# Performance work log

Measured on AMD Instinct MI355X. Metric: run time of the kernel, lower is better.

Reference implementation:

```python
import jax, jax.numpy as jnp
import numpy as np

EMB_DIM = 64
B, S, D = 64, 1024, 64

def setup_inputs() -> dict:
    key = jax.random.key(0)
    k1, k2, k3, k4, k5 = jax.random.split(key, 5)
    return {
        "query": jax.random.normal(k1, (B, S, D), dtype=jnp.float32),
        "key": jax.random.normal(k2, (B, S, D), dtype=jnp.float32),
        "value": jax.random.normal(k3, (B, S, D), dtype=jnp.float32),
        "a_key": jax.random.normal(k4, (S, S, D), dtype=jnp.float32),
        "a_value": jax.random.normal(k5, (S, S, D), dtype=jnp.float32),
    }

def reference(query, key, value, a_key, a_value):
    scale = jnp.sqrt(jnp.asarray(EMB_DIM, dtype=query.dtype))
    # standard content-content scores: [B, Sq, Sk]
    qk = jnp.einsum("bqd,bkd->bqk", query, key)
    # relative key scores: a_key is [Sq, Sk, D]; contract over D per query position
    rel_qk = jnp.einsum("bqd,qkd->bqk", query, a_key)
    attn = jax.nn.softmax((qk + rel_qk) / scale, axis=-1)
    # content values + relative values
    qkv = jnp.einsum("bqk,bkd->bqd", attn, value)
    rel_qkv = jnp.einsum("bqk,qkd->bqd", attn, a_value)
    return qkv + rel_qkv, attn
```

## Files before the change

kernel.cpp:

```cpp
#include <hip/hip_runtime.h>
#include <stdint.h>

#define S_ 1024
#define D_ 64
#define B_ 64

typedef short short8 __attribute__((ext_vector_type(8)));
typedef unsigned short ushort8 __attribute__((ext_vector_type(8)));
typedef float f32x4 __attribute__((ext_vector_type(4)));
typedef unsigned short u16;

__device__ __forceinline__ u16 f2bf(float x) {
    uint32_t u = __builtin_bit_cast(uint32_t, x);
    return (u16)((u + 0x7FFFu + ((u >> 16) & 1u)) >> 16);
}
__device__ __forceinline__ float bf2f(u16 b) {
    return __builtin_bit_cast(float, ((uint32_t)b) << 16);
}
__device__ __forceinline__ uint32_t pack2(float a, float b) {
    return (uint32_t)f2bf(a) | ((uint32_t)f2bf(b) << 16);
}
__device__ __forceinline__ int scidx(int row, int k) {
    return (((row << 10) + (k & ~7)) ^ ((row & 15) << 3)) + (k & 7);
}

template <int WS>
__global__ __launch_bounds__(256) void k1_qk(const float* __restrict__ Q,
                                             const float* __restrict__ Kk,
                                             float* __restrict__ qkf,
                                             u16* __restrict__ qkb) {
    __shared__ __align__(16) u16 Qs[128][72];
    __shared__ __align__(16) u16 Ks[128][72];
    const float SCL = 0.18033688011112042f;
    const int bx = blockIdx.x;
    const int b  = bx >> 6;
    const int q0 = ((bx >> 3) & 7) << 7;
    const int k0 = (bx & 7) << 7;
    const int t  = threadIdx.x;
#pragma unroll
    for (int i = 0; i < 8; ++i) {
        int f = (i << 8) + t;
        int row = f >> 4, c = (f & 15) << 2;
        float4 v = *reinterpret_cast<const float4*>(&Q[((size_t)(b * S_ + q0 + row) << 6) + c]);
        *reinterpret_cast<uint2*>(&Qs[row][c]) = make_uint2(pack2(v.x, v.y), pack2(v.z, v.w));
        float4 u = *reinterpret_cast<const float4*>(&Kk[((size_t)(b * S_ + k0 + row) << 6) + c]);
        *reinterpret_cast<uint2*>(&Ks[row][c]) = make_uint2(pack2(u.x, u.y), pack2(u.z, u.w));
    }
    __syncthreads();
    const int l = t & 63, w = t >> 6, lr = l & 15, lg = l >> 4;
    short8 a[2][2];
#pragma unroll
    for (int mi = 0; mi < 2; ++mi)
#pragma unroll
        for (int h = 0; h < 2; ++h)
            a[mi][h] = *reinterpret_cast<const short8*>(&Qs[((w * 2 + mi) << 4) + lr][h * 32 + lg * 8]);
    f32x4 acc[2][8] = {};
#pragma unroll
    for (int n = 0; n < 8; ++n) {
        short8 b0 = *reinterpret_cast<const short8*>(&Ks[(n << 4) + lr][lg * 8]);
        short8 b1 = *reinterpret_cast<const short8*>(&Ks[(n << 4) + lr][32 + lg * 8]);
#pragma unroll
        for (int mi = 0; mi < 2; ++mi) {
            acc[mi][n] = __builtin_amdgcn_mfma_f32_16x16x32_bf16(a[mi][0], b0, acc[mi][n], 0, 0, 0);
            acc[mi][n] = __builtin_amdgcn_mfma_f32_16x16x32_bf16(a[mi][1], b1, acc[mi][n], 0, 0, 0);
        }
    }
#pragma unroll
    for (int mi = 0; mi < 2; ++mi)
#pragma unroll
        for (int n = 0; n < 8; ++n)
#pragma unroll
            for (int r = 0; r < 4; ++r) {
                int qq = q0 + ((w * 2 + mi) << 4) + (lg << 2) + r;
                int kc = k0 + (n << 4) + lr;
                size_t idx = ((size_t)(b * S_ + qq) << 10) + kc;
                if (WS) qkb[idx] = f2bf(acc[mi][n][r] * SCL);
                else    qkf[idx] = acc[mi][n][r] * SCL;
            }
}

__device__ __forceinline__ void tpose_store_p(u16* Tls, int pitch, float4 p,
                                              int kb, int t) {
    const int l = t & 63, lr = l & 15, lg = l >> 4;
    float v0 = p.x, v1 = p.y, v2 = p.z, v3 = p.w;
    float y0 = __shfl_xor(v0, 16), y1 = __shfl_xor(v1, 16),
          y2 = __shfl_xor(v2, 16), y3 = __shfl_xor(v3, 16);
    bool o = (lg & 1);
    float n0 = o ? y1 : v0, n1 = o ? v1 : y0, n2 = o ? y3 : v2, n3 = o ? v3 : y2;
    float z0 = __shfl_xor(n0, 32), z1 = __shfl_xor(n1, 32),
          z2 = __shfl_xor(n2, 32), z3 = __shfl_xor(n3, 32);
    bool h = (lg & 2);
    float T0 = h ? z2 : n0, T1 = h ? z3 : n1, T2 = h ? n2 : z0, T3 = h ? n3 : z1;
    int d = (lr << 2) + lg;
    *reinterpret_cast<uint2*>(&Tls[d * pitch + kb]) = make_uint2(pack2(T0, T1), pack2(T2, T3));
}

template <int WS>
__global__ __launch_bounds__(512) void k2_mid(const float* __restrict__ Q,
                                              const float* __restrict__ AK,
                                              const float* __restrict__ AV,
                                              const u16* __restrict__ qkb,
                                              const float* __restrict__ qkf,
                                              float* __restrict__ attn,
                                              float* __restrict__ outp) {
    __shared__ __align__(16) u16 Sc[64 * 1024];
    __shared__ __align__(16) u16 Qs[64][72];
    __shared__ __align__(16) u16 Ak[2][64][72];
    __shared__ float invs[64];
    const float SCL = 0.18033688011112042f;
    const int q = blockIdx.x;
    const int t = threadIdx.x;
    const int l = t & 63, w = t >> 6, lr = l & 15, lg = l >> 4;
    const int wq = w & 3;
    const int wh = w >> 2;
    const int srow = t >> 3, sc8 = (t & 7) << 3;

    {
        const float* qp = &Q[((size_t)(srow * S_ + q) << 6) + sc8];
        float4 a = *reinterpret_cast<const float4*>(qp);
        float4 b = *reinterpret_cast<const float4*>(qp + 4);
        *reinterpret_cast<uint4*>(&Qs[srow][sc8]) =
            make_uint4(pack2(a.x * SCL, a.y * SCL), pack2(a.z * SCL, a.w * SCL),
                       pack2(b.x * SCL, b.y * SCL), pack2(b.z * SCL, b.w * SCL));
    }
    const float* akbase = &AK[(size_t)q << 16];
    float4 pa[2][2];
#define LDK(set, tile) do { const float* p_ = akbase + ((size_t)(tile) << 12) + (srow << 6) + sc8; \
        pa[set][0] = *reinterpret_cast<const float4*>(p_);                                         \
        pa[set][1] = *reinterpret_cast<const float4*>(p_ + 4); } while (0)
#define STAGEK(buf) do {                                                                     \
        *reinterpret_cast<uint4*>(&Ak[buf][srow][sc8]) =                                     \
            make_uint4(pack2(pa[buf][0].x, pa[buf][0].y), pack2(pa[buf][0].z, pa[buf][0].w), \
                       pack2(pa[buf][1].x, pa[buf][1].y), pack2(pa[buf][1].z, pa[buf][1].w)); } while (0)
    LDK(0, 0); LDK(1, 1);
    __syncthreads();
    short8 qa[2][2];
#pragma unroll
    for (int bh = 0; bh < 2; ++bh)
#pragma unroll
        for (int h = 0; h < 2; ++h)
            qa[bh][h] = *reinterpret_cast<const short8*>(
                &Qs[(wh << 5) + (bh << 4) + lr][(h << 5) + (lg << 3)]);
    STAGEK(0);
    __syncthreads();

#pragma unroll 2
    for (int tt = 0; tt < 16; ++tt) {
        const int cur = tt & 1, nxt = cur ^ 1;
        short8 ak0 = *reinterpret_cast<const short8*>(&Ak[cur][(wq << 4) + lr][lg << 3]);
        short8 ak1 = *reinterpret_cast<const short8*>(&Ak[cur][(wq << 4) + lr][32 + (lg << 3)]);
        if (tt < 15) STAGEK(nxt);
        if (tt < 14) LDK(cur, tt + 2);
        int kbase = (tt << 6) + (wq << 4) + (lg << 2);
#pragma unroll
        for (int bh = 0; bh < 2; ++bh) {
            f32x4 c = {};
            c = __builtin_amdgcn_mfma_f32_16x16x32_bf16(ak0, qa[bh][0], c, 0, 0, 0);
            c = __builtin_amdgcn_mfma_f32_16x16x32_bf16(ak1, qa[bh][1], c, 0, 0, 0);
            *reinterpret_cast<uint2*>(&Sc[scidx((wh << 5) + (bh << 4) + lr, kbase)]) =
                make_uint2(pack2(c[0], c[1]), pack2(c[2], c[3]));
        }
        __syncthreads();
    }
#undef LDK
#undef STAGEK

    const float* avbase = &AV[(size_t)q << 16];
    float4 pv[2][2];
#pragma unroll
    for (int s = 0; s < 2; ++s)
#pragma unroll
        for (int i = 0; i < 2; ++i) {
            int f = (i << 9) + t;
            pv[s][i] = *reinterpret_cast<const float4*>(
                &avbase[((size_t)s << 12) + ((size_t)(f >> 4) << 6) + ((f & 15) << 2)]);
        }

    {
        const int ch = t & 7;
        float s = 0.f;
#pragma unroll 4
        for (int i = 0; i < 16; ++i) {
            int k = (((i << 3) + ch) << 3);
            int idx = scidx(srow, k);
            ushort8 rel = *reinterpret_cast<const ushort8*>(&Sc[idx]);
            float g[8];
            if (WS) {
                ushort8 gq = *reinterpret_cast<const ushort8*>(
                    &qkb[((size_t)(srow * S_ + q) << 10) + k]);
#pragma unroll
                for (int jj = 0; jj < 8; ++jj) g[jj] = bf2f(gq[jj]);
            } else {
                const float* qkrow = &qkf[((size_t)(srow * S_ + q) << 10)];
                float4 g0 = *reinterpret_cast<const float4*>(&qkrow[k]);
                float4 g1 = *reinterpret_cast<const float4*>(&qkrow[k + 4]);
                g[0] = g0.x; g[1] = g0.y; g[2] = g0.z; g[3] = g0.w;
                g[4] = g1.x; g[5] = g1.y; g[6] = g1.z; g[7] = g1.w;
            }
            ushort8 e;
#pragma unroll
            for (int jj = 0; jj < 8; ++jj) {
                float ev = exp2f(g[jj] + bf2f(rel[jj]));
                s += ev;
                e[jj] = f2bf(ev);
            }
            *reinterpret_cast<ushort8*>(&Sc[idx]) = e;
        }
        s += __shfl_xor(s, 1); s += __shfl_xor(s, 2); s += __shfl_xor(s, 4);
        if (ch == 0) invs[srow] = 1.0f / s;
    }
    __syncthreads();

    tpose_store_p(&Ak[0][0][0], 72, pv[0][0], (w << 2), t);
    tpose_store_p(&Ak[0][0][0], 72, pv[0][1], 32 + (w << 2), t);
    __syncthreads();

    f32x4 oacc[2] = {};
#pragma unroll 2
    for (int tt = 0; tt < 16; ++tt) {
        const int cur = tt & 1, nxt = cur ^ 1;
        short8 bb0 = *reinterpret_cast<const short8*>(&Ak[cur][(wq << 4) + lr][lg << 3]);
        short8 bb1 = *reinterpret_cast<const short8*>(&Ak[cur][(wq << 4) + lr][32 + (lg << 3)]);
        if (tt < 15) {
            tpose_store_p(&Ak[nxt][0][0], 72, pv[nxt][0], (w << 2), t);
            tpose_store_p(&Ak[nxt][0][0], 72, pv[nxt][1], 32 + (w << 2), t);
        }
        if (tt < 14) {
#pragma unroll
            for (int i = 0; i < 2; ++i) {
                int f = (i << 9) + t;
                pv[cur][i] = *reinterpret_cast<const float4*>(
                    &avbase[((size_t)(tt + 2) << 12) + ((size_t)(f >> 4) << 6) + ((f & 15) << 2)]);
            }
        }
        {
            int col = (t & 255) << 2;
#pragma unroll
            for (int rr = 0; rr < 2; ++rr) {
                int row = (tt << 2) + (rr << 1) + (t >> 8);
                uint2 u = *reinterpret_cast<const uint2*>(&Sc[scidx(row, col)]);
                float inv = invs[row];
                float4 o = make_float4(bf2f((u16)(u.x & 0xffff)) * inv,
                                       bf2f((u16)(u.x >> 16)) * inv,
                                       bf2f((u16)(u.y & 0xffff)) * inv,
                                       bf2f((u16)(u.y >> 16)) * inv);
                *reinterpret_cast<float4*>(&attn[((size_t)(row * S_ + q) << 10) + col]) = o;
            }
        }
#pragma unroll
        for (int mi = 0; mi < 2; ++mi) {
            short8 ea0 = *reinterpret_cast<const short8*>(
                &Sc[scidx((wh << 5) + (mi << 4) + lr, (tt << 6) + (lg << 3))]);
            short8 ea1 = *reinterpret_cast<const short8*>(
                &Sc[scidx((wh << 5) + (mi << 4) + lr, (tt << 6) + 32 + (lg << 3))]);
            oacc[mi] = __builtin_amdgcn_mfma_f32_16x16x32_bf16(ea0, bb0, oacc[mi], 0, 0, 0);
            oacc[mi] = __builtin_amdgcn_mfma_f32_16x16x32_bf16(ea1, bb1, oacc[mi], 0, 0, 0);
        }
        __syncthreads();
    }
#pragma unroll
    for (int mi = 0; mi < 2; ++mi)
#pragma unroll
        for (int r = 0; r < 4; ++r) {
            int brow = (wh << 5) + (mi << 4) + (lg << 2) + r;
            outp[((size_t)(brow * S_ + q) << 6) + (wq << 4) + lr] = oacc[mi][r] * invs[brow];
        }
}

__global__ __launch_bounds__(512) void k3_pv(const float* __restrict__ V,
                                             const float* __restrict__ attn,
                                             float* __restrict__ outp) {
    __shared__ __align__(16) u16 Vt[64 * 1032];
    __shared__ __align__(16) u16 At[2][64][72];
    const int b  = blockIdx.x >> 2;
    const int qq = blockIdx.x & 3;
    const int t  = threadIdx.x;
    const int l = t & 63, w = t >> 6, lr = l & 15, lg = l >> 4;
    const int wq = w & 3;
    const int dh = w >> 2;
    const int srow = t >> 3, sc8 = (t & 7) << 3;

    for (int kt = 0; kt < 16; ++kt) {
#pragma unroll
        for (int i = 0; i < 2; ++i) {
            int f = (i << 9) + t;
            int row = f >> 4, c = (f & 15) << 2;
            float4 pvv = *reinterpret_cast<const float4*>(
                &V[((size_t)(b * S_ + (kt << 6) + row) << 6) + c]);
            tpose_store_p(&Vt[0], 1032, pvv, (kt << 6) + (i << 5) + (w << 2), t);
        }
    }
    __syncthreads();

    for (int qs = 0; qs < 4; ++qs) {
        const float* arow = &attn[((size_t)((b * S_ + (qq << 8) + (qs << 6) + srow)) << 10) + sc8];
        float4 pa[2][2];
#define LDA3(set, tile) do { const float* p_ = arow + ((tile) << 6);       \
        pa[set][0] = *reinterpret_cast<const float4*>(p_);                 \
        pa[set][1] = *reinterpret_cast<const float4*>(p_ + 4); } while (0)
#define STAGEA(buf) do {                                                                     \
        *reinterpret_cast<uint4*>(&At[buf][srow][sc8]) =                                     \
            make_uint4(pack2(pa[buf][0].x, pa[buf][0].y), pack2(pa[buf][0].z, pa[buf][0].w), \
                       pack2(pa[buf][1].x, pa[buf][1].y), pack2(pa[buf][1].z, pa[buf][1].w)); } while (0)
        LDA3(0, 0); LDA3(1, 1);
        __syncthreads();
        STAGEA(0);
        __syncthreads();
        f32x4 acc[2] = {};
#pragma unroll 2
        for (int kt = 0; kt < 16; ++kt) {
            const int cur = kt & 1, nxt = cur ^ 1;
            short8 a0 = *reinterpret_cast<const short8*>(&At[cur][(wq << 4) + lr][lg << 3]);
            short8 a1 = *reinterpret_cast<const short8*>(&At[cur][(wq << 4) + lr][32 + (lg << 3)]);
            if (kt < 15) STAGEA(nxt);
            if (kt < 14) LDA3(cur, kt + 2);
#pragma unroll
            for (int n = 0; n < 2; ++n) {
                const u16* vb = &Vt[((dh << 5) + (n << 4) + lr) * 1032 + (kt << 6) + (lg << 3)];
                short8 b0 = *reinterpret_cast<const short8*>(vb);
                short8 b1 = *reinterpret_cast<const short8*>(vb + 32);
                acc[n] = __builtin_amdgcn_mfma_f32_16x16x32_bf16(a0, b0, acc[n], 0, 0, 0);
                acc[n] = __builtin_amdgcn_mfma_f32_16x16x32_bf16(a1, b1, acc[n], 0, 0, 0);
            }
            __syncthreads();
        }
#undef LDA3
#undef STAGEA
#pragma unroll
        for (int n = 0; n < 2; ++n)
#pragma unroll
            for (int r = 0; r < 4; ++r) {
                size_t idx = ((size_t)(b * S_ + (qq << 8) + (qs << 6) + (wq << 4) + (lg << 2) + r) << 6)
                             + (dh << 5) + (n << 4) + lr;
                outp[idx] += acc[n][r];
            }
    }
}

extern "C" void kernel_launch(void* const* d_in, const int* in_sizes, int n_in,
                              void* d_out, int out_size, void* d_ws, size_t ws_size,
                              hipStream_t stream) {
    (void)in_sizes; (void)n_in; (void)out_size;
    const float* Q  = (const float*)d_in[0];
    const float* K  = (const float*)d_in[1];
    const float* V  = (const float*)d_in[2];
    const float* AK = (const float*)d_in[3];
    const float* AV = (const float*)d_in[4];
    float* outp = (float*)d_out;
    float* attn = outp + (size_t)B_ * S_ * D_;
    u16*   qkb  = (u16*)d_ws;
    const size_t qk_bytes = (size_t)B_ * S_ * S_ * sizeof(u16);

    if (ws_size >= qk_bytes) {
        k1_qk<1> <<<dim3(64 * 8 * 8), dim3(256), 0, stream>>>(Q, K, attn, qkb);
        k2_mid<1><<<dim3(1024),       dim3(512), 0, stream>>>(Q, AK, AV, qkb, attn, attn, outp);
    } else {
        k1_qk<0> <<<dim3(64 * 8 * 8), dim3(256), 0, stream>>>(Q, K, attn, qkb);
        k2_mid<0><<<dim3(1024),       dim3(512), 0, stream>>>(Q, AK, AV, qkb, attn, attn, outp);
    }
    k3_pv<<<dim3(256), dim3(512), 0, stream>>>(V, attn, outp);
}
```

Measured before the change: 353.0 us.

## Pass unnormalized bf16 probabilities via workspace and move attn writeout to k3

k2 now writes its unnormalized bf16 exp scores back into the qk workspace in place, plus per-row inverse sums, and no longer writes the fp32 attn matrix. k3 reads the bf16 probabilities directly as MFMA A-operands from global memory, dropping the LDS staging and its barriers. It writes the normalized fp32 attn rows itself and scales its output by the inverse sums. This replaces an fp32 attn write plus fp32 read-back with a bf16 write plus read, cutting global traffic, in exchange for more work in k3 and a somewhat larger workspace requirement.

```diff
diff --git a/kernel.cpp b/kernel.cpp
--- a/kernel.cpp
+++ b/kernel.cpp
@@ -99,8 +99,9 @@
 __global__ __launch_bounds__(512) void k2_mid(const float* __restrict__ Q,
                                               const float* __restrict__ AK,
                                               const float* __restrict__ AV,
-                                              const u16* __restrict__ qkb,
+                                              u16* __restrict__ qkb,
                                               const float* __restrict__ qkf,
+                                              float* __restrict__ invg,
                                               float* __restrict__ attn,
                                               float* __restrict__ outp) {
     __shared__ __align__(16) u16 Sc[64 * 1024];
@@ -205,9 +206,15 @@
                 e[jj] = f2bf(ev);
             }
             *reinterpret_cast<ushort8*>(&Sc[idx]) = e;
+            if (WS)
+                *reinterpret_cast<ushort8*>(&qkb[((size_t)(srow * S_ + q) << 10) + k]) = e;
         }
         s += __shfl_xor(s, 1); s += __shfl_xor(s, 2); s += __shfl_xor(s, 4);
-        if (ch == 0) invs[srow] = 1.0f / s;
+        if (ch == 0) {
+            float inv = 1.0f / s;
+            invs[srow] = inv;
+            if (WS) invg[srow * S_ + q] = inv;
+        }
     }
     __syncthreads();
 
@@ -233,7 +240,7 @@
                     &avbase[((size_t)(tt + 2) << 12) + ((size_t)(f >> 4) << 6) + ((f & 15) << 2)]);
             }
         }
-        {
+        if (!WS) {
             int col = (t & 255) << 2;
 #pragma unroll
             for (int rr = 0; rr < 2; ++rr) {
@@ -267,8 +274,11 @@
         }
 }
 
+template <int WS>
 __global__ __launch_bounds__(512) void k3_pv(const float* __restrict__ V,
-                                             const float* __restrict__ attn,
+                                             float* __restrict__ attn,
+                                             const u16* __restrict__ P,
+                                             const float* __restrict__ invg,
                                              float* __restrict__ outp) {
     __shared__ __align__(16) u16 Vt[64 * 1032];
     __shared__ __align__(16) u16 At[2][64][72];
@@ -293,47 +303,98 @@
     __syncthreads();
 
     for (int qs = 0; qs < 4; ++qs) {
-        const float* arow = &attn[((size_t)((b * S_ + (qq << 8) + (qs << 6) + srow)) << 10) + sc8];
-        float4 pa[2][2];
+        const int qsbase = (qq << 8) + (qs << 6);
+        f32x4 acc[2] = {};
+        if (WS) {
+            const u16* prow = &P[((size_t)(b * S_ + qsbase + (wq << 4) + lr) << 10) + (lg << 3)];
+            short8 a0b[2], a1b[2];
+#define LDPB(buf, kt) do { const u16* p_ = prow + ((kt) << 6);              \
+            a0b[buf] = *reinterpret_cast<const short8*>(p_);                \
+            a1b[buf] = *reinterpret_cast<const short8*>(p_ + 32); } while (0)
+            LDPB(0, 0); LDPB(1, 1);
+#pragma unroll 2
+            for (int kt = 0; kt < 16; ++kt) {
+                const int buf = kt & 1;
+                short8 a0 = a0b[buf], a1 = a1b[buf];
+                if (kt < 14) LDPB(buf, kt + 2);
+                {
+                    int col = (t & 255) << 2;
+#pragma unroll
+                    for (int rr = 0; rr < 2; ++rr) {
+                        int row = qsbase + (kt << 2) + (rr << 1) + (t >> 8);
+                        uint2 u = *reinterpret_cast<const uint2*>(
+                            &P[((size_t)(b * S_ + row) << 10) + col]);
+                        float inv = invg[b * S_ + row];
+                        float4 o = make_float4(bf2f((u16)(u.x & 0xffff)) * inv,
+                                               bf2f((u16)(u.x >> 16)) * inv,
+                                               bf2f((u16)(u.y & 0xffff)) * inv,
+                                               bf2f((u16)(u.y >> 16)) * inv);
+                        *reinterpret_cast<float4*>(&attn[((size_t)(b * S_ + row) << 10) + col]) = o;
+                    }
+                }
+#pragma unroll
+                for (int n = 0; n < 2; ++n) {
+                    const u16* vb = &Vt[((dh << 5) + (n << 4) + lr) * 1032 + (kt << 6) + (lg << 3)];
+                    short8 b0 = *reinterpret_cast<const short8*>(vb);
+                    short8 b1 = *reinterpret_cast<const short8*>(vb + 32);
+                    acc[n] = __builtin_amdgcn_mfma_f32_16x16x32_bf16(a0, b0, acc[n], 0, 0, 0);
+                    acc[n] = __builtin_amdgcn_mfma_f32_16x16x32_bf16(a1, b1, acc[n], 0, 0, 0);
+                }
+            }
+#undef LDPB
+            float4 inv4 = *reinterpret_cast<const float4*>(
+                &invg[b * S_ + qsbase + (wq << 4) + (lg << 2)]);
+            float invr[4] = {inv4.x, inv4.y, inv4.z, inv4.w};
+#pragma unroll
+            for (int n = 0; n < 2; ++n)
+#pragma unroll
+                for (int r = 0; r < 4; ++r) {
+                    size_t idx = ((size_t)(b * S_ + qsbase + (wq << 4) + (lg << 2) + r) << 6)
+                                 + (dh << 5) + (n << 4) + lr;
+                    outp[idx] += acc[n][r] * invr[r];
+                }
+        } else {
+            const float* arow = &attn[((size_t)(b * S_ + qsbase + srow) << 10) + sc8];
+            float4 pa[2][2];
 #define LDA3(set, tile) do { const float* p_ = arow + ((tile) << 6);       \
-        pa[set][0] = *reinterpret_cast<const float4*>(p_);                 \
-        pa[set][1] = *reinterpret_cast<const float4*>(p_ + 4); } while (0)
+            pa[set][0] = *reinterpret_cast<const float4*>(p_);             \
+            pa[set][1] = *reinterpret_cast<const float4*>(p_ + 4); } while (0)
 #define STAGEA(buf) do {                                                                     \
-        *reinterpret_cast<uint4*>(&At[buf][srow][sc8]) =                                     \
-            make_uint4(pack2(pa[buf][0].x, pa[buf][0].y), pack2(pa[buf][0].z, pa[buf][0].w), \
-                       pack2(pa[buf][1].x, pa[buf][1].y), pack2(pa[buf][1].z, pa[buf][1].w)); } while (0)
-        LDA3(0, 0); LDA3(1, 1);
-        __syncthreads();
-        STAGEA(0);
-        __syncthreads();
-        f32x4 acc[2] = {};
+            *reinterpret_cast<uint4*>(&At[buf][srow][sc8]) =                                 \
+                make_uint4(pack2(pa[buf][0].x, pa[buf][0].y), pack2(pa[buf][0].z, pa[buf][0].w), \
+                           pack2(pa[buf][1].x, pa[buf][1].y), pack2(pa[buf][1].z, pa[buf][1].w)); } while (0)
+            LDA3(0, 0); LDA3(1, 1);
+            __syncthreads();
+            STAGEA(0);
+            __syncthreads();
 #pragma unroll 2
-        for (int kt = 0; kt < 16; ++kt) {
-            const int cur = kt & 1, nxt = cur ^ 1;
-            short8 a0 = *reinterpret_cast<const short8*>(&At[cur][(wq << 4) + lr][lg << 3]);
-            short8 a1 = *reinterpret_cast<const short8*>(&At[cur][(wq << 4) + lr][32 + (lg << 3)]);
-            if (kt < 15) STAGEA(nxt);
-            if (kt < 14) LDA3(cur, kt + 2);
-#pragma unroll
-            for (int n = 0; n < 2; ++n) {
-                const u16* vb = &Vt[((dh << 5) + (n << 4) + lr) * 1032 + (kt << 6) + (lg << 3)];
-                short8 b0 = *reinterpret_cast<const short8*>(vb);
-                short8 b1 = *reinterpret_cast<const short8*>(vb + 32);
-                acc[n] = __builtin_amdgcn_mfma_f32_16x16x32_bf16(a0, b0, acc[n], 0, 0, 0);
-                acc[n] = __builtin_amdgcn_mfma_f32_16x16x32_bf16(a1, b1, acc[n], 0, 0, 0);
-            }
-            __syncthreads();
-        }
+            for (int kt = 0; kt < 16; ++kt) {
+                const int cur = kt & 1, nxt = cur ^ 1;
+                short8 a0 = *reinterpret_cast<const short8*>(&At[cur][(wq << 4) + lr][lg << 3]);
+                short8 a1 = *reinterpret_cast<const short8*>(&At[cur][(wq << 4) + lr][32 + (lg << 3)]);
+                if (kt < 15) STAGEA(nxt);
+                if (kt < 14) LDA3(cur, kt + 2);
+#pragma unroll
+                for (int n = 0; n < 2; ++n) {
+                    const u16* vb = &Vt[((dh << 5) + (n << 4) + lr) * 1032 + (kt << 6) + (lg << 3)];
+                    short8 b0 = *reinterpret_cast<const short8*>(vb);
+                    short8 b1 = *reinterpret_cast<const short8*>(vb + 32);
+                    acc[n] = __builtin_amdgcn_mfma_f32_16x16x32_bf16(a0, b0, acc[n], 0, 0, 0);
+                    acc[n] = __builtin_amdgcn_mfma_f32_16x16x32_bf16(a1, b1, acc[n], 0, 0, 0);
+                }
+                __syncthreads();
+            }
 #undef LDA3
 #undef STAGEA
 #pragma unroll
-        for (int n = 0; n < 2; ++n)
-#pragma unroll
-            for (int r = 0; r < 4; ++r) {
-                size_t idx = ((size_t)(b * S_ + (qq << 8) + (qs << 6) + (wq << 4) + (lg << 2) + r) << 6)
-                             + (dh << 5) + (n << 4) + lr;
-                outp[idx] += acc[n][r];
-            }
+            for (int n = 0; n < 2; ++n)
+#pragma unroll
+                for (int r = 0; r < 4; ++r) {
+                    size_t idx = ((size_t)(b * S_ + qsbase + (wq << 4) + (lg << 2) + r) << 6)
+                                 + (dh << 5) + (n << 4) + lr;
+                    outp[idx] += acc[n][r];
+                }
+        }
     }
 }
 
@@ -349,14 +410,17 @@
     float* outp = (float*)d_out;
     float* attn = outp + (size_t)B_ * S_ * D_;
     u16*   qkb  = (u16*)d_ws;
-    const size_t qk_bytes = (size_t)B_ * S_ * S_ * sizeof(u16);
-
-    if (ws_size >= qk_bytes) {
+    float* invg = (float*)(qkb + (size_t)B_ * S_ * S_);
+    const size_t need = (size_t)B_ * S_ * S_ * sizeof(u16)
+                      + (size_t)B_ * S_ * sizeof(float);
+
+    if (ws_size >= need) {
         k1_qk<1> <<<dim3(64 * 8 * 8), dim3(256), 0, stream>>>(Q, K, attn, qkb);
-        k2_mid<1><<<dim3(1024),       dim3(512), 0, stream>>>(Q, AK, AV, qkb, attn, attn, outp);
+        k2_mid<1><<<dim3(1024),       dim3(512), 0, stream>>>(Q, AK, AV, qkb, attn, invg, attn, outp);
+        k3_pv<1> <<<dim3(256),        dim3(512), 0, stream>>>(V, attn, qkb, invg, outp);
     } else {
         k1_qk<0> <<<dim3(64 * 8 * 8), dim3(256), 0, stream>>>(Q, K, attn, qkb);
-        k2_mid<0><<<dim3(1024),       dim3(512), 0, stream>>>(Q, AK, AV, qkb, attn, attn, outp);
-    }
-    k3_pv<<<dim3(256), dim3(512), 0, stream>>>(V, attn, outp);
-}
+        k2_mid<0><<<dim3(1024),       dim3(512), 0, stream>>>(Q, AK, AV, qkb, attn, invg, attn, outp);
+        k3_pv<0> <<<dim3(256),        dim3(512), 0, stream>>>(V, attn, qkb, invg, outp);
+    }
+}
```

New measurement: 373.4 us. 5.8% more time.
